# Optimization experiments

Measured on AMD Instinct MI355X. Metric: run time of the kernel, lower is better.

## Reference

```python
import jax, jax.numpy as jnp
import numpy as np

B, L, H, NUM_LABELS = 4, 256, 768, 13


def setup_inputs() -> dict:
    key = jax.random.key(0)
    k1, k2, k3, k4, k5 = jax.random.split(key, 5)
    s1 = 1.0 / np.sqrt(2 * H)
    s2 = 1.0 / np.sqrt(H)
    return {
        "hidden_states": jax.random.normal(k1, (B, L, H), dtype=jnp.float32),
        "W1": jax.random.uniform(k2, (2 * H, H), jnp.float32, -s1, s1),
        "b1": jax.random.uniform(k3, (H,), jnp.float32, -s1, s1),
        "W2": jax.random.uniform(k4, (H, NUM_LABELS), jnp.float32, -s2, s2),
        "b2": jax.random.uniform(k5, (NUM_LABELS,), jnp.float32, -s2, s2),
    }


def reference(hidden_states, W1, b1, W2, b2):
    # Original: ffn(cat([x_start expand over dim2, x_end expand over dim1], -1))
    # Algebraically: Linear(2H->H) on the concat == proj(x_start) + proj(x_end)
    # broadcast over the L x L span grid, avoiding the (B,L,L,2H) tensor.
    H_ = hidden_states.shape[-1]
    xs_proj = jnp.einsum('bsh,hk->bsk', hidden_states, W1[:H_])   # start half
    xe_proj = jnp.einsum('bsh,hk->bsk', hidden_states, W1[H_:])   # end half
    h = xs_proj[:, :, None, :] + xe_proj[:, None, :, :] + b1      # (B,L,L,H)
    h = jax.nn.gelu(h, approximate=False)                         # torch GELU default = exact erf
    logits = jnp.einsum('bijk,kn->bijn', h, W2) + b2              # (B,L,L,num_labels)
    return logits
```

## Files before the change

kernel.cpp:

```cpp
#include <hip/hip_runtime.h>
#include <math.h>

#define H 768
#define L 256
#define NB 4
#define NL 13

typedef _Float16 h2 __attribute__((ext_vector_type(2)));
typedef _Float16 half8 __attribute__((ext_vector_type(8)));
typedef float f32x4 __attribute__((ext_vector_type(4)));

__device__ inline h2 gelu_pk(h2 x) {
    const _Float16 kC = (_Float16)3.75f;
    h2 hi = {kC, kC}, lo = {(_Float16)-3.75f, (_Float16)-3.75f};
    h2 xc = __builtin_elementwise_min(__builtin_elementwise_max(x, lo), hi);
    h2 u = xc * xc;
    const _Float16 kE = (_Float16)0.125f;
    h2 ve = {kE, kE};
    h2 v = u * ve;
    const _Float16 d4v = (_Float16)0.0832840f,  d3v = (_Float16)-0.4335206f;
    const _Float16 d2v = (_Float16)0.8960128f,  d1v = (_Float16)-0.9876456f;
    const _Float16 d0v = (_Float16)0.7946463f;
    h2 d4 = {d4v, d4v}, d3 = {d3v, d3v}, d2 = {d2v, d2v}, d1 = {d1v, d1v}, d0 = {d0v, d0v};
    h2 p = v * (v * (v * (v * d4 + d3) + d2) + d1) + d0;
    h2 t = xc * p;
    const _Float16 kH = (_Float16)0.5f;
    h2 halfv = {kH, kH};
    h2 hx = x * halfv;
    return hx * t + hx;
}

__global__ __launch_bounds__(256) void prep_kernel(
    const float* __restrict__ X, const float* __restrict__ W1,
    const float* __restrict__ W2,
    _Float16* __restrict__ Afrag, _Float16* __restrict__ Bfrag1,
    _Float16* __restrict__ Bfrag2)
{
    const int blk = blockIdx.x;
    const int tid = threadIdx.x;

    if (blk < 384) {
        int t = blk * 256 + tid;
        int lane = t & 63;
        int g = t >> 6;
        int kb = g % 24, mt = g / 24;
        int m = mt * 16 + (lane & 15);
        int k0 = kb * 32 + (lane >> 4) * 8;
        const float* px = X + (size_t)m * H + k0;
        float4 a = *(const float4*)px;
        float4 b = *(const float4*)(px + 4);
        half8 o = { (_Float16)a.x, (_Float16)a.y, (_Float16)a.z, (_Float16)a.w,
                    (_Float16)b.x, (_Float16)b.y, (_Float16)b.z, (_Float16)b.w };
        *(half8*)(Afrag + (size_t)t * 8) = o;
    } else if (blk < 960) {
        int t = (blk - 384) * 256 + tid;
        int lane = t & 63;
        int g = t >> 6;
        int kb = g % 24, ntg = g / 24;
        int np = ntg * 16 + (lane & 15);
        int k0 = kb * 32 + (lane >> 4) * 8;
        const float* Wb = W1 + ((np >= H) ? (size_t)H * H : 0);
        int c = np - ((np >= H) ? H : 0);
        half8 o;
        #pragma unroll
        for (int u = 0; u < 8; ++u)
            o[u] = (_Float16)Wb[(size_t)(k0 + u) * H + c];
        *(half8*)(Bfrag1 + (size_t)t * 8) = o;
    } else {
        int base = (blk - 960) * 768 + tid;
        #pragma unroll
        for (int r = 0; r < 3; ++r) {
            int idx = base + r * 256;
            int u = idx & 7;
            int lane = (idx >> 3) & 63;
            int kb = idx >> 9;
            int k = kb * 32 + ((lane >> 4) << 3) + u;
            int n = lane & 15;
            float v = (n < NL) ? W2[(size_t)k * NL + n] : 0.f;
            Bfrag2[idx] = (_Float16)v;
        }
    }
}

__global__ __launch_bounds__(256) void gemm_mfma(
    const _Float16* __restrict__ Afrag, const _Float16* __restrict__ Bfrag1,
    const float* __restrict__ b1, _Float16* __restrict__ Pxs2,
    _Float16* __restrict__ Pxe)
{
    const int tid = threadIdx.x;
    const int w = tid >> 6, lane = tid & 63;
    const int ln = lane & 15, quad = lane >> 4;
    const int m0 = blockIdx.x * 64 + (w & 1) * 32;
    const int n0g = blockIdx.y * 64 + (w >> 1) * 32;
    const int mt0 = m0 >> 4, ntg0 = n0g >> 4;

    const half8* pa0 = (const half8*)(Afrag + (((size_t)mt0 * 24) * 64 + lane) * 8);
    const half8* pa1 = (const half8*)(Afrag + ((((size_t)mt0 + 1) * 24) * 64 + lane) * 8);
    const half8* pb0 = (const half8*)(Bfrag1 + (((size_t)ntg0 * 24) * 64 + lane) * 8);
    const half8* pb1 = (const half8*)(Bfrag1 + ((((size_t)ntg0 + 1) * 24) * 64 + lane) * 8);

    f32x4 acc[2][2] = {};
    #pragma unroll 4
    for (int kb = 0; kb < 24; ++kb) {
        half8 a0 = pa0[kb * 64];
        half8 a1 = pa1[kb * 64];
        half8 b0 = pb0[kb * 64];
        half8 b1v = pb1[kb * 64];
        acc[0][0] = __builtin_amdgcn_mfma_f32_16x16x32_f16(a0, b0, acc[0][0], 0, 0, 0);
        acc[0][1] = __builtin_amdgcn_mfma_f32_16x16x32_f16(a0, b1v, acc[0][1], 0, 0, 0);
        acc[1][0] = __builtin_amdgcn_mfma_f32_16x16x32_f16(a1, b0, acc[1][0], 0, 0, 0);
        acc[1][1] = __builtin_amdgcn_mfma_f32_16x16x32_f16(a1, b1v, acc[1][1], 0, 0, 0);
    }

    if (n0g < H) {
        float bv[2] = { b1[n0g + ln], b1[n0g + 16 + ln] };
        #pragma unroll
        for (int mt = 0; mt < 2; ++mt)
            #pragma unroll
            for (int nt = 0; nt < 2; ++nt) {
                int n = n0g + nt * 16 + ln;
                #pragma unroll
                for (int r = 0; r < 4; ++r) {
                    int m = m0 + mt * 16 + quad * 4 + r;
                    Pxs2[(size_t)m * H + n] = (_Float16)(acc[mt][nt][r] + bv[nt]);
                }
            }
    } else {
        #pragma unroll
        for (int mt = 0; mt < 2; ++mt)
            #pragma unroll
            for (int nt = 0; nt < 2; ++nt) {
                int n = n0g - H + nt * 16 + ln;
                #pragma unroll
                for (int r = 0; r < 4; ++r) {
                    int m = m0 + mt * 16 + quad * 4 + r;
                    Pxe[(size_t)m * H + n] = (_Float16)acc[mt][nt][r];
                }
            }
    }
}

__global__ __launch_bounds__(256, 4) void span_mfma_kernel(
    const _Float16* __restrict__ Pxs2, const _Float16* __restrict__ Pxe,
    const _Float16* __restrict__ Bfrag2, const float* __restrict__ b2,
    float* __restrict__ out)
{
    __shared__ unsigned int xsf[2 * H / 2];
    const int ip = blockIdx.x >> 2;
    const int jq = blockIdx.x & 3;
    const int bi0 = ip * 2;
    const int b = bi0 >> 8;
    const int tid = threadIdx.x;

    const unsigned int* xsrc = (const unsigned int*)(Pxs2 + (size_t)bi0 * H);
    for (int t = tid; t < H; t += 256) xsf[t] = xsrc[t];

    const int wave = tid >> 6;
    const int lane = tid & 63;
    const int n = lane & 15;
    const int quad = lane >> 4;
    const int j_load = jq * 64 + wave * 16 + n;

    const _Float16* xerow = Pxe + (size_t)(b * L + j_load) * H + quad * 8;
    const half8* bptr = (const half8*)(Bfrag2 + (size_t)lane * 8);

    f32x4 acc[2] = {};
    __syncthreads();

    for (int kb = 0; kb < H / 32; ++kb) {
        half8 bfrag = bptr[kb * 64];
        uint4 xev = *(const uint4*)(xerow + kb * 32);
        h2 xep[4] = { __builtin_bit_cast(h2, xev.x), __builtin_bit_cast(h2, xev.y),
                      __builtin_bit_cast(h2, xev.z), __builtin_bit_cast(h2, xev.w) };
        const int xo = kb * 16 + quad * 4;

        #pragma unroll
        for (int i01 = 0; i01 < 2; ++i01) {
            uint4 xsd = *(const uint4*)&xsf[i01 * (H / 2) + xo];
            h2 xsp[4] = { __builtin_bit_cast(h2, xsd.x), __builtin_bit_cast(h2, xsd.y),
                          __builtin_bit_cast(h2, xsd.z), __builtin_bit_cast(h2, xsd.w) };
            unsigned int pk[4];
            #pragma unroll
            for (int p = 0; p < 4; ++p) {
                h2 g = gelu_pk(xsp[p] + xep[p]);
                pk[p] = __builtin_bit_cast(unsigned int, g);
            }
            uint4 pk4 = {pk[0], pk[1], pk[2], pk[3]};
            half8 afrag = __builtin_bit_cast(half8, pk4);
            acc[i01] = __builtin_amdgcn_mfma_f32_16x16x32_f16(afrag, bfrag, acc[i01], 0, 0, 0);
        }
    }

    if (n < NL) {
        float b2v = b2[n];
        #pragma unroll
        for (int i01 = 0; i01 < 2; ++i01)
            #pragma unroll
            for (int r = 0; r < 4; ++r) {
                int j = jq * 64 + wave * 16 + quad * 4 + r;
                out[((size_t)(bi0 + i01) * L + j) * NL + n] = acc[i01][r] + b2v;
            }
    }
}

extern "C" void kernel_launch(void* const* d_in, const int* in_sizes, int n_in,
                              void* d_out, int out_size, void* d_ws, size_t ws_size,
                              hipStream_t stream)
{
    (void)in_sizes; (void)n_in; (void)out_size; (void)ws_size;
    const float* X  = (const float*)d_in[0];
    const float* W1 = (const float*)d_in[1];
    const float* b1 = (const float*)d_in[2];
    const float* W2 = (const float*)d_in[3];
    const float* b2 = (const float*)d_in[4];
    float* out = (float*)d_out;

    char* ws = (char*)d_ws;
    _Float16* Pxs2   = (_Float16*)ws;
    _Float16* Pxe    = Pxs2 + (size_t)NB * L * H;
    _Float16* Afrag  = Pxe + (size_t)NB * L * H;
    _Float16* Bfrag1 = Afrag + (size_t)NB * L * H;
    _Float16* Bfrag2 = Bfrag1 + (size_t)2 * H * H;

    prep_kernel<<<976, 256, 0, stream>>>(X, W1, W2, Afrag, Bfrag1, Bfrag2);
    gemm_mfma<<<dim3(16, 24), 256, 0, stream>>>(Afrag, Bfrag1, b1, Pxs2, Pxe);
    span_mfma_kernel<<<NB * L * 2, 256, 0, stream>>>(Pxs2, Pxe, Bfrag2, b2, out);
}
```

Baseline: 124.6 us.

## Fuse prep, projection GEMM and span kernel into one cooperative persistent kernel

```diff
diff --git a/kernel.cpp b/kernel.cpp
--- a/kernel.cpp
+++ b/kernel.cpp
@@ -1,5 +1,8 @@
 #include <hip/hip_runtime.h>
+#include <hip/hip_cooperative_groups.h>
 #include <math.h>
+
+namespace cg = cooperative_groups;
 
 #define H 768
 #define L 256
@@ -30,176 +33,166 @@
     return hx * t + hx;
 }
 
-__global__ __launch_bounds__(256) void prep_kernel(
+__global__ __launch_bounds__(256, 4) void mono_kernel(
     const float* __restrict__ X, const float* __restrict__ W1,
-    const float* __restrict__ W2,
+    const float* __restrict__ b1, const float* __restrict__ W2,
+    const float* __restrict__ b2,
     _Float16* __restrict__ Afrag, _Float16* __restrict__ Bfrag1,
-    _Float16* __restrict__ Bfrag2)
+    _Float16* __restrict__ Bfrag2,
+    _Float16* __restrict__ Pxs2, _Float16* __restrict__ Pxe,
+    float* __restrict__ out)
 {
+    cg::grid_group grid = cg::this_grid();
     const int blk = blockIdx.x;
     const int tid = threadIdx.x;
-
-    if (blk < 384) {
+    const int lane = tid & 63;
+    const int wave = tid >> 6;
+    const int ln = lane & 15, quad = lane >> 4;
+
+    __shared__ unsigned int xsf[2 * H / 2];
+
+    {
         int t = blk * 256 + tid;
-        int lane = t & 63;
-        int g = t >> 6;
-        int kb = g % 24, mt = g / 24;
-        int m = mt * 16 + (lane & 15);
-        int k0 = kb * 32 + (lane >> 4) * 8;
-        const float* px = X + (size_t)m * H + k0;
-        float4 a = *(const float4*)px;
-        float4 b = *(const float4*)(px + 4);
-        half8 o = { (_Float16)a.x, (_Float16)a.y, (_Float16)a.z, (_Float16)a.w,
-                    (_Float16)b.x, (_Float16)b.y, (_Float16)b.z, (_Float16)b.w };
-        *(half8*)(Afrag + (size_t)t * 8) = o;
-    } else if (blk < 960) {
-        int t = (blk - 384) * 256 + tid;
-        int lane = t & 63;
-        int g = t >> 6;
-        int kb = g % 24, ntg = g / 24;
-        int np = ntg * 16 + (lane & 15);
-        int k0 = kb * 32 + (lane >> 4) * 8;
-        const float* Wb = W1 + ((np >= H) ? (size_t)H * H : 0);
-        int c = np - ((np >= H) ? H : 0);
-        half8 o;
-        #pragma unroll
-        for (int u = 0; u < 8; ++u)
-            o[u] = (_Float16)Wb[(size_t)(k0 + u) * H + c];
-        *(half8*)(Bfrag1 + (size_t)t * 8) = o;
-    } else {
-        int base = (blk - 960) * 768 + tid;
-        #pragma unroll
-        for (int r = 0; r < 3; ++r) {
-            int idx = base + r * 256;
+        if (t < 98304) {
+            int l = t & 63;
+            int g = t >> 6;
+            int kb = g % 24, mt = g / 24;
+            int m = mt * 16 + (l & 15);
+            int k0 = kb * 32 + (l >> 4) * 8;
+            const float* px = X + (size_t)m * H + k0;
+            float4 a = *(const float4*)px;
+            float4 c = *(const float4*)(px + 4);
+            half8 o = { (_Float16)a.x, (_Float16)a.y, (_Float16)a.z, (_Float16)a.w,
+                        (_Float16)c.x, (_Float16)c.y, (_Float16)c.z, (_Float16)c.w };
+            *(half8*)(Afrag + (size_t)t * 8) = o;
+        } else if (t < 245760) {
+            int t2 = t - 98304;
+            int l = t2 & 63;
+            int g = t2 >> 6;
+            int kb = g % 24, ntg = g / 24;
+            int np = ntg * 16 + (l & 15);
+            int k0 = kb * 32 + (l >> 4) * 8;
+            const float* Wb = W1 + ((np >= H) ? (size_t)H * H : 0);
+            int c = np - ((np >= H) ? H : 0);
+            half8 o;
+            #pragma unroll
+            for (int u = 0; u < 8; ++u)
+                o[u] = (_Float16)Wb[(size_t)(k0 + u) * H + c];
+            *(half8*)(Bfrag1 + (size_t)t2 * 8) = o;
+        } else if (t < 258048) {
+            int idx = t - 245760;
             int u = idx & 7;
-            int lane = (idx >> 3) & 63;
+            int l = (idx >> 3) & 63;
             int kb = idx >> 9;
-            int k = kb * 32 + ((lane >> 4) << 3) + u;
-            int n = lane & 15;
+            int k = kb * 32 + ((l >> 4) << 3) + u;
+            int n = l & 15;
             float v = (n < NL) ? W2[(size_t)k * NL + n] : 0.f;
             Bfrag2[idx] = (_Float16)v;
         }
     }
-}
-
-__global__ __launch_bounds__(256) void gemm_mfma(
-    const _Float16* __restrict__ Afrag, const _Float16* __restrict__ Bfrag1,
-    const float* __restrict__ b1, _Float16* __restrict__ Pxs2,
-    _Float16* __restrict__ Pxe)
-{
-    const int tid = threadIdx.x;
-    const int w = tid >> 6, lane = tid & 63;
-    const int ln = lane & 15, quad = lane >> 4;
-    const int m0 = blockIdx.x * 64 + (w & 1) * 32;
-    const int n0g = blockIdx.y * 64 + (w >> 1) * 32;
-    const int mt0 = m0 >> 4, ntg0 = n0g >> 4;
-
-    const half8* pa0 = (const half8*)(Afrag + (((size_t)mt0 * 24) * 64 + lane) * 8);
-    const half8* pa1 = (const half8*)(Afrag + ((((size_t)mt0 + 1) * 24) * 64 + lane) * 8);
-    const half8* pb0 = (const half8*)(Bfrag1 + (((size_t)ntg0 * 24) * 64 + lane) * 8);
-    const half8* pb1 = (const half8*)(Bfrag1 + ((((size_t)ntg0 + 1) * 24) * 64 + lane) * 8);
-
-    f32x4 acc[2][2] = {};
-    #pragma unroll 4
-    for (int kb = 0; kb < 24; ++kb) {
-        half8 a0 = pa0[kb * 64];
-        half8 a1 = pa1[kb * 64];
-        half8 b0 = pb0[kb * 64];
-        half8 b1v = pb1[kb * 64];
-        acc[0][0] = __builtin_amdgcn_mfma_f32_16x16x32_f16(a0, b0, acc[0][0], 0, 0, 0);
-        acc[0][1] = __builtin_amdgcn_mfma_f32_16x16x32_f16(a0, b1v, acc[0][1], 0, 0, 0);
-        acc[1][0] = __builtin_amdgcn_mfma_f32_16x16x32_f16(a1, b0, acc[1][0], 0, 0, 0);
-        acc[1][1] = __builtin_amdgcn_mfma_f32_16x16x32_f16(a1, b1v, acc[1][1], 0, 0, 0);
-    }
-
-    if (n0g < H) {
-        float bv[2] = { b1[n0g + ln], b1[n0g + 16 + ln] };
-        #pragma unroll
-        for (int mt = 0; mt < 2; ++mt)
-            #pragma unroll
-            for (int nt = 0; nt < 2; ++nt) {
-                int n = n0g + nt * 16 + ln;
-                #pragma unroll
-                for (int r = 0; r < 4; ++r) {
-                    int m = m0 + mt * 16 + quad * 4 + r;
-                    Pxs2[(size_t)m * H + n] = (_Float16)(acc[mt][nt][r] + bv[nt]);
+    grid.sync();
+
+    {
+        int wj = blk * 4 + wave;
+        if (wj < 3072) {
+            int mt = wj / 48;
+            int p  = wj % 48;
+            int ntg0 = p * 2;
+
+            const half8* pa  = (const half8*)(Afrag + (((size_t)mt * 24) * 64 + lane) * 8);
+            const half8* pb0 = (const half8*)(Bfrag1 + (((size_t)ntg0 * 24) * 64 + lane) * 8);
+            const half8* pb1 = pb0 + (size_t)24 * 64;
+
+            f32x4 acc[2] = {};
+            #pragma unroll 4
+            for (int kb = 0; kb < 24; ++kb) {
+                half8 a  = pa[kb * 64];
+                half8 b0 = pb0[kb * 64];
+                half8 b1v = pb1[kb * 64];
+                acc[0] = __builtin_amdgcn_mfma_f32_16x16x32_f16(a, b0, acc[0], 0, 0, 0);
+                acc[1] = __builtin_amdgcn_mfma_f32_16x16x32_f16(a, b1v, acc[1], 0, 0, 0);
+            }
+
+            if (p < 24) {
+                #pragma unroll
+                for (int nt = 0; nt < 2; ++nt) {
+                    int np = (ntg0 + nt) * 16 + ln;
+                    float bv = b1[np];
+                    #pragma unroll
+                    for (int r = 0; r < 4; ++r) {
+                        int m = mt * 16 + quad * 4 + r;
+                        Pxs2[(size_t)m * H + np] = (_Float16)(acc[nt][r] + bv);
+                    }
                 }
-            }
-    } else {
-        #pragma unroll
-        for (int mt = 0; mt < 2; ++mt)
-            #pragma unroll
-            for (int nt = 0; nt < 2; ++nt) {
-                int n = n0g - H + nt * 16 + ln;
-                #pragma unroll
-                for (int r = 0; r < 4; ++r) {
-                    int m = m0 + mt * 16 + quad * 4 + r;
-                    Pxe[(size_t)m * H + n] = (_Float16)acc[mt][nt][r];
+            } else {
+                #pragma unroll
+                for (int nt = 0; nt < 2; ++nt) {
+                    int np = (ntg0 + nt) * 16 + ln - H;
+                    #pragma unroll
+                    for (int r = 0; r < 4; ++r) {
+                        int m = mt * 16 + quad * 4 + r;
+                        Pxe[(size_t)m * H + np] = (_Float16)acc[nt][r];
+                    }
                 }
             }
-    }
-}
-
-__global__ __launch_bounds__(256, 4) void span_mfma_kernel(
-    const _Float16* __restrict__ Pxs2, const _Float16* __restrict__ Pxe,
-    const _Float16* __restrict__ Bfrag2, const float* __restrict__ b2,
-    float* __restrict__ out)
-{
-    __shared__ unsigned int xsf[2 * H / 2];
-    const int ip = blockIdx.x >> 2;
-    const int jq = blockIdx.x & 3;
-    const int bi0 = ip * 2;
-    const int b = bi0 >> 8;
-    const int tid = threadIdx.x;
-
-    const unsigned int* xsrc = (const unsigned int*)(Pxs2 + (size_t)bi0 * H);
-    for (int t = tid; t < H; t += 256) xsf[t] = xsrc[t];
-
-    const int wave = tid >> 6;
-    const int lane = tid & 63;
-    const int n = lane & 15;
-    const int quad = lane >> 4;
-    const int j_load = jq * 64 + wave * 16 + n;
-
-    const _Float16* xerow = Pxe + (size_t)(b * L + j_load) * H + quad * 8;
-    const half8* bptr = (const half8*)(Bfrag2 + (size_t)lane * 8);
-
-    f32x4 acc[2] = {};
-    __syncthreads();
-
-    for (int kb = 0; kb < H / 32; ++kb) {
-        half8 bfrag = bptr[kb * 64];
-        uint4 xev = *(const uint4*)(xerow + kb * 32);
-        h2 xep[4] = { __builtin_bit_cast(h2, xev.x), __builtin_bit_cast(h2, xev.y),
-                      __builtin_bit_cast(h2, xev.z), __builtin_bit_cast(h2, xev.w) };
-        const int xo = kb * 16 + quad * 4;
-
-        #pragma unroll
-        for (int i01 = 0; i01 < 2; ++i01) {
-            uint4 xsd = *(const uint4*)&xsf[i01 * (H / 2) + xo];
-            h2 xsp[4] = { __builtin_bit_cast(h2, xsd.x), __builtin_bit_cast(h2, xsd.y),
-                          __builtin_bit_cast(h2, xsd.z), __builtin_bit_cast(h2, xsd.w) };
-            unsigned int pk[4];
-            #pragma unroll
-            for (int p = 0; p < 4; ++p) {
-                h2 g = gelu_pk(xsp[p] + xep[p]);
-                pk[p] = __builtin_bit_cast(unsigned int, g);
-            }
-            uint4 pk4 = {pk[0], pk[1], pk[2], pk[3]};
-            half8 afrag = __builtin_bit_cast(half8, pk4);
-            acc[i01] = __builtin_amdgcn_mfma_f32_16x16x32_f16(afrag, bfrag, acc[i01], 0, 0, 0);
         }
     }
-
-    if (n < NL) {
-        float b2v = b2[n];
+    grid.sync();
+
+    {
+        const int ip = blk >> 1;
+        const int bi0 = ip * 2;
+        const int b = bi0 >> 8;
+        const unsigned int* xsrc = (const unsigned int*)(Pxs2 + (size_t)bi0 * H);
+        for (int t = tid; t < H; t += 256) xsf[t] = xsrc[t];
+        __syncthreads();
+
+        const int n = ln;
+        const int jq0 = (blk & 1) * 2;
+        const half8* bptr = (const half8*)(Bfrag2 + (size_t)lane * 8);
+        const float b2v = (n < NL) ? b2[n] : 0.f;
+
         #pragma unroll
-        for (int i01 = 0; i01 < 2; ++i01)
-            #pragma unroll
-            for (int r = 0; r < 4; ++r) {
-                int j = jq * 64 + wave * 16 + quad * 4 + r;
-                out[((size_t)(bi0 + i01) * L + j) * NL + n] = acc[i01][r] + b2v;
-            }
+        for (int rep = 0; rep < 2; ++rep) {
+            const int jq = jq0 + rep;
+            const int j_load = jq * 64 + wave * 16 + n;
+            const _Float16* xerow = Pxe + (size_t)(b * L + j_load) * H + quad * 8;
+
+            f32x4 acc[2] = {};
+            for (int kb = 0; kb < H / 32; ++kb) {
+                half8 bfrag = bptr[kb * 64];
+                uint4 xev = *(const uint4*)(xerow + kb * 32);
+                h2 xep[4] = { __builtin_bit_cast(h2, xev.x), __builtin_bit_cast(h2, xev.y),
+                              __builtin_bit_cast(h2, xev.z), __builtin_bit_cast(h2, xev.w) };
+                const int xo = kb * 16 + quad * 4;
+
+                #pragma unroll
+                for (int i01 = 0; i01 < 2; ++i01) {
+                    uint4 xsd = *(const uint4*)&xsf[i01 * (H / 2) + xo];
+                    h2 xsp[4] = { __builtin_bit_cast(h2, xsd.x), __builtin_bit_cast(h2, xsd.y),
+                                  __builtin_bit_cast(h2, xsd.z), __builtin_bit_cast(h2, xsd.w) };
+                    unsigned int pk[4];
+                    #pragma unroll
+                    for (int pp = 0; pp < 4; ++pp) {
+                        h2 g = gelu_pk(xsp[pp] + xep[pp]);
+                        pk[pp] = __builtin_bit_cast(unsigned int, g);
+                    }
+                    uint4 pk4 = {pk[0], pk[1], pk[2], pk[3]};
+                    half8 afrag = __builtin_bit_cast(half8, pk4);
+                    acc[i01] = __builtin_amdgcn_mfma_f32_16x16x32_f16(afrag, bfrag, acc[i01], 0, 0, 0);
+                }
+            }
+
+            if (n < NL) {
+                #pragma unroll
+                for (int i01 = 0; i01 < 2; ++i01)
+                    #pragma unroll
+                    for (int r = 0; r < 4; ++r) {
+                        int j = jq * 64 + wave * 16 + quad * 4 + r;
+                        out[((size_t)(bi0 + i01) * L + j) * NL + n] = acc[i01][r] + b2v;
+                    }
+            }
+        }
     }
 }
 
@@ -222,7 +215,9 @@
     _Float16* Bfrag1 = Afrag + (size_t)NB * L * H;
     _Float16* Bfrag2 = Bfrag1 + (size_t)2 * H * H;
 
-    prep_kernel<<<976, 256, 0, stream>>>(X, W1, W2, Afrag, Bfrag1, Bfrag2);
-    gemm_mfma<<<dim3(16, 24), 256, 0, stream>>>(Afrag, Bfrag1, b1, Pxs2, Pxe);
-    span_mfma_kernel<<<NB * L * 2, 256, 0, stream>>>(Pxs2, Pxe, Bfrag2, b2, out);
+    void* args[] = { (void*)&X, (void*)&W1, (void*)&b1, (void*)&W2, (void*)&b2,
+                     (void*)&Afrag, (void*)&Bfrag1, (void*)&Bfrag2,
+                     (void*)&Pxs2, (void*)&Pxe, (void*)&out };
+    hipLaunchCooperativeKernel((const void*)mono_kernel, dim3(1024), dim3(256),
+                               args, 0, stream);
 }
```

After: 337.0 us. +170.5%, slower.
